# Kernel tuning notes

Hardware: AMD Instinct MI355X
Metric: run time of the kernel (lower is better)

Reference implementation:

```python
import jax, jax.numpy as jnp
import numpy as np

N, CS, CZ, H, C, PQ, PV, N0, N1 = 768, 384, 128, 12, 64, 4, 8, 192, 64
CZ4 = CZ // 4
INF, EPS = 1e5, 1e-8


def setup_inputs() -> dict:
    key = jax.random.key(0)
    ks = jax.random.split(key, 24)

    def w(k, i, o):
        return jax.random.normal(k, (i, o), jnp.float32) / np.float32(np.sqrt(i))

    s = jax.random.normal(ks[0], (N, CS), jnp.float32)
    z = jax.random.normal(ks[1], (N, N, CZ), jnp.float32)
    rot = jnp.linalg.qr(jax.random.normal(ks[2], (N, 3, 3), jnp.float32))[0]
    trans = jax.random.normal(ks[3], (N, 3), jnp.float32)
    mask = jnp.ones((N,), jnp.float32)
    is_atom = jax.random.bernoulli(ks[4], 0.5, (N,))
    return dict(
        s=s, z=z, rot=rot, trans=trans, mask=mask, is_atom=is_atom,
        wq=w(ks[5], CS, H * C), bq=jnp.zeros((H * C,), jnp.float32),
        wkv=w(ks[6], CS, 2 * H * C), bkv=jnp.zeros((2 * H * C,), jnp.float32),
        wqp=w(ks[7], CS, 3 * H * PQ), bqp=jnp.zeros((3 * H * PQ,), jnp.float32),
        wkvp=w(ks[8], CS, 3 * H * (PQ + PV)), bkvp=jnp.zeros((3 * H * (PQ + PV),), jnp.float32),
        wb=w(ks[9], CZ, H), bb=jnp.zeros((H,), jnp.float32),
        wdz=w(ks[10], CZ, CZ4), bdz=jnp.zeros((CZ4,), jnp.float32),
        head_weights=jnp.full((H,), 0.5413248, jnp.float32),  # softplus^-1(1), per ipa_point_weights_init_
        wout=w(ks[11], H * (C + 4 * PV + CZ4), CS), bout=jnp.zeros((CS,), jnp.float32),
        tfnq_ws=w(ks[12], N0, H * C), tfnq_wv=w(ks[13], N1, H * PQ),
        tfnkv_ws=w(ks[14], N0, 2 * H * C), tfnkv_wv=w(ks[15], N1, H * (PQ + PV)),
        tfno_ws=w(ks[16], H * (C + PV + CZ4), N0), tfno_wv=w(ks[17], H * PV, N1),
    )


def reference(s, z, rot, trans, mask, is_atom, wq, bq, wkv, bkv, wqp, bqp, wkvp, bkvp,
              wb, bb, wdz, bdz, head_weights, wout, bout,
              tfnq_ws, tfnq_wv, tfnkv_ws, tfnkv_wv, tfno_ws, tfno_wv):
    n = s.shape[0]

    def apply_rigid(pts):  # pts: [n, P, 3] -> R x + t
        return jnp.einsum('nij,npj->npi', rot, pts) + trans[:, None, :]

    # ---- residue (frame) path ----
    q_r = (s @ wq + bq).reshape(n, H, C)
    kv_r = (s @ wkv + bkv).reshape(n, H, 2 * C)
    k_r, v_r = kv_r[..., :C], kv_r[..., C:]
    # torch.split-in-3 then stack(dim=-1) layout: [n, 3, H*P] -> [n, H*P, 3]
    qp = (s @ wqp + bqp).reshape(n, 3, H * PQ).transpose(0, 2, 1)
    q_pts_r = apply_rigid(qp).reshape(n, H, PQ, 3)
    kvp = (s @ wkvp + bkvp).reshape(n, 3, H * (PQ + PV)).transpose(0, 2, 1)
    kv_pts_r = apply_rigid(kvp).reshape(n, H, PQ + PV, 3)
    k_pts_r, v_pts_r = kv_pts_r[..., :PQ, :], kv_pts_r[..., PQ:, :]

    # ---- atom (TFN-equivariant) path: irreps = N0 scalars + N1 vectors ----
    sc = s[:, :N0]
    vec = s[:, N0:N0 + 3 * N1].reshape(n, N1, 3)
    q_a = (sc @ tfnq_ws).reshape(n, H, C)
    q_pts_a = jnp.einsum('nix,io->nox', vec, tfnq_wv).reshape(n, H, PQ, 3) + trans[:, None, None, :]
    kv_a = (sc @ tfnkv_ws).reshape(n, H, 2 * C)
    k_a, v_a = kv_a[..., :C], kv_a[..., C:]
    kv_pts_a = jnp.einsum('nix,io->nox', vec, tfnkv_wv).reshape(n, H, PQ + PV, 3) + trans[:, None, None, :]
    k_pts_a, v_pts_a = kv_pts_a[..., :PQ, :], kv_pts_a[..., PQ:, :]

    m1 = is_atom[:, None, None]
    m2 = is_atom[:, None, None, None]
    q = jnp.where(m1, q_a, q_r)
    k = jnp.where(m1, k_a, k_r)
    v = jnp.where(m1, v_a, v_r)
    q_pts = jnp.where(m2, q_pts_a, q_pts_r)
    k_pts = jnp.where(m2, k_pts_a, k_pts_r)
    v_pts = jnp.where(m2, v_pts_a, v_pts_r)

    # ---- attention logits ----
    b = z @ wb + bb  # [n, n, H]
    a = jnp.einsum('nhc,mhc->hnm', q, k) * np.float32(np.sqrt(1.0 / (3 * C)))
    a = a + np.float32(np.sqrt(1.0 / 3)) * b.transpose(2, 0, 1)

    disp = q_pts[:, None] - k_pts[None]          # [n, n, H, PQ, 3]
    pt_att = jnp.sum(disp * disp, axis=-1)       # [n, n, H, PQ]
    hw = jax.nn.softplus(head_weights) * np.float32(np.sqrt(1.0 / (3 * (PQ * 9.0 / 2))))
    pt_att = -0.5 * jnp.sum(pt_att * hw[:, None], axis=-1)  # [n, n, H]
    a = a + pt_att.transpose(2, 0, 1)

    sq_mask = INF * (mask[:, None] * mask[None, :] - 1.0)
    a = jax.nn.softmax(a + sq_mask[None], axis=-1)  # [H, n, n]

    # ---- aggregation ----
    o = jnp.einsum('hnm,mhc->nhc', a, v).reshape(n, H * C)
    o_pt = jnp.einsum('hnm,mhpx->nhpx', a, v_pts)  # [n, H, PV, 3]
    o_pt = jnp.einsum('nji,nhpj->nhpi', rot, o_pt - trans[:, None, None, :])  # invert_apply
    o_pt_norm = jnp.sqrt(jnp.sum(o_pt * o_pt, axis=-1) + EPS).reshape(n, H * PV)
    o_pt = o_pt.reshape(n, H * PV, 3)
    pair_z = z @ wdz + bdz  # [n, n, CZ4]
    o_pair = jnp.einsum('hnm,nmz->nhz', a, pair_z).reshape(n, H * CZ4)

    # ---- residue output head ----
    res_feats = jnp.concatenate([o, o_pt[..., 0], o_pt[..., 1], o_pt[..., 2], o_pt_norm, o_pair], axis=-1)
    res_out = res_feats @ wout + bout  # [n, CS]

    # ---- atom output head (equivariant linear: scalars mix, vectors mix per-component) ----
    atom_sc = jnp.concatenate([o, o_pt_norm, o_pair], axis=-1) @ tfno_ws  # [n, N0]
    atom_vec = jnp.einsum('npx,po->nox', o_pt, tfno_wv).reshape(n, 3 * N1)
    atom_out = jnp.concatenate([atom_sc, atom_vec], axis=-1)  # [n, CS]

    return jnp.where(is_atom[:, None], atom_out, res_out)
```

## Files before the change

kernel.cpp:

```cpp
#include <hip/hip_runtime.h>
#include <hip/hip_bf16.h>

static constexpr int NN = 768;

typedef short v8bf __attribute__((ext_vector_type(8)));
typedef float v4f  __attribute__((ext_vector_type(4)));
typedef unsigned short ushort_t;

__device__ __forceinline__ unsigned short f2bf(float f) {
  unsigned u = __float_as_uint(f);
  u += 0x7fffu + ((u >> 16) & 1u);
  return (unsigned short)(u >> 16);
}
__device__ __forceinline__ float bf2f(unsigned short s) {
  return __uint_as_float(((unsigned)s) << 16);
}

static constexpr size_t OFF_ISA    = 0;
static constexpr size_t OFF_WCT    = 1024;
static constexpr size_t OFF_BCAT   = 4096;
static constexpr size_t OFF_SBF    = 4160;
static constexpr size_t OFF_WQT    = 151616;
static constexpr size_t OFF_WKVT   = 299072;
static constexpr size_t OFF_WQPT   = 593984;
static constexpr size_t OFF_WKVPT  = 630848;
static constexpr size_t OFF_TFNQT  = 716864;
static constexpr size_t OFF_TFNKVT = 815168;
static constexpr size_t OFF_WOUTT  = 1011776;
static constexpr size_t OFF_TFNOT  = 1306688;
static constexpr size_t OFF_QR     = 1429568;
static constexpr size_t OFF_KVR    = 1724480;
static constexpr size_t OFF_QP     = 2314304;
static constexpr size_t OFF_KVP    = 2424896;
static constexpr size_t OFF_QA     = 2756672;
static constexpr size_t OFF_KVA    = 3051584;
static constexpr size_t OFF_QCAT   = 3641408;
static constexpr size_t OFF_KCAT   = 4083776;
static constexpr size_t OFF_RQ     = 4526144;
static constexpr size_t OFF_RK     = 4535360;
static constexpr size_t OFF_VCATN  = 4544576;
static constexpr size_t OFF_VCATT  = 4986944;
static constexpr size_t OFF_BB     = 5429312;
static constexpr size_t OFF_PZT    = 8968256;
static constexpr size_t OFF_ABF    = 18405440;
static constexpr size_t OFF_OPTRAW = 21944384;
static constexpr size_t OFF_RESF   = 22165568;
static constexpr size_t OFF_ATOMF  = 22755392;

__device__ void transpose_cv(const float* __restrict__ src, unsigned short* __restrict__ dst,
                             int K, int Kp, int N, int ky, int nx) {
  __shared__ float tl[32][33];
  const int k0 = ky * 32, n0 = nx * 32;
  const int tx = threadIdx.x & 31, ty = threadIdx.x >> 5;
  for (int it = 0; it < 4; ++it) {
    int r = ty + it * 8;
    float v = 0.f;
    if (k0 + r < K && n0 + tx < N) v = src[(long long)(k0 + r) * N + n0 + tx];
    tl[r][tx] = v;
  }
  __syncthreads();
  for (int it = 0; it < 4; ++it) {
    int r = ty + it * 8;
    if (n0 + r < N && k0 + tx < Kp)
      dst[(long long)(n0 + r) * Kp + k0 + tx] = f2bf(tl[tx][r]);
  }
}

__global__ __launch_bounds__(256) void prep0(
    float* wsf, const float* s, const float* wq, const float* wkv,
    const float* wqp, const float* wkvp, const float* tfnq_ws,
    const float* tfnkv_ws, const float* wout, const float* tfno_ws,
    const float* wb, const float* wdz, const float* bb, const float* bdz,
    const unsigned int* isa_raw)
{
  const int bx = blockIdx.x, t = threadIdx.x;
  if (bx < 288)       { int g = bx;        transpose_cv(wq,      (unsigned short*)(wsf+OFF_WQT),    384, 384, 768,  g/24, g%24); return; }
  else if (bx < 864)  { int g = bx-288;    transpose_cv(wkv,     (unsigned short*)(wsf+OFF_WKVT),   384, 384, 1536, g/48, g%48); return; }
  else if (bx < 924)  { int g = bx-864;    transpose_cv(wqp,     (unsigned short*)(wsf+OFF_WQPT),   384, 384, 144,  g/5,  g%5);  return; }
  else if (bx < 1092) { int g = bx-924;    transpose_cv(wkvp,    (unsigned short*)(wsf+OFF_WKVPT),  384, 384, 432,  g/14, g%14); return; }
  else if (bx < 1284) { int g = bx-1092;   transpose_cv(tfnq_ws, (unsigned short*)(wsf+OFF_TFNQT),  192, 256, 768,  g/24, g%24); return; }
  else if (bx < 1668) { int g = bx-1284;   transpose_cv(tfnkv_ws,(unsigned short*)(wsf+OFF_TFNKVT), 192, 256, 1536, g/48, g%48); return; }
  else if (bx < 2244) { int g = bx-1668;   transpose_cv(wout,    (unsigned short*)(wsf+OFF_WOUTT),  1536,1536,384,  g/12, g%12); return; }
  else if (bx < 2484) { int g = bx-2244;   transpose_cv(tfno_ws, (unsigned short*)(wsf+OFF_TFNOT),  1248,1280,192,  g/6,  g%6);  return; }
  else if (bx < 2772) {
    long long base = (long long)(bx - 2484) * 1024 + t * 4;
    float4 v = *(const float4*)(s + base);
    unsigned short tmp[4] = {f2bf(v.x), f2bf(v.y), f2bf(v.z), f2bf(v.w)};
    *(uint2*)((unsigned short*)(wsf + OFF_SBF) + base) = *(uint2*)tmp;
    return;
  } else if (bx < 2773) {
    __shared__ int notint, notfloat;
    int* ISA = (int*)(wsf + OFF_ISA);
    if (t == 0) { notint = 0; notfloat = 0; }
    __syncthreads();
    if (t < 192) {
      unsigned v = isa_raw[t];
      if (v > 1u) atomicOr(&notint, 1);
      if (v != 0u && v != 0x3F800000u) atomicOr(&notfloat, 1);
    }
    __syncthreads();
    const int mode = (!notint) ? 0 : ((!notfloat) ? 1 : 2);
    for (int n = t; n < NN; n += 256) {
      int val;
      if (mode == 2) val = (((const unsigned char*)isa_raw)[n] != 0);
      else           val = (isa_raw[n] != 0u);
      ISA[n] = val;
    }
    return;
  } else {
    const float rs3 = 0.57735026918962576f;
    unsigned short* WCT = (unsigned short*)(wsf + OFF_WCT);
    float* bcat = wsf + OFF_BCAT;
    int idx = (bx - 2773) * 256 + t;
    if (idx < 48 * 128) {
      int o = idx >> 7, k = idx & 127;
      float v = 0.f;
      if (o < 12) v = rs3 * wb[k * 12 + o];
      else if (o < 44) v = wdz[k * 32 + (o - 12)];
      WCT[o * 128 + k] = f2bf(v);
    }
    if (bx == 2773 && t < 48)
      bcat[t] = (t < 12) ? rs3 * bb[t] : (t < 44 ? bdz[t - 12] : 0.f);
  }
}

__device__ __forceinline__ void gemm16(
    char* lds, const unsigned short* __restrict__ A, int lda,
    const unsigned short* __restrict__ BT, int ldb, int KQ,
    const float* __restrict__ bias, int mode,
    float* Cf, unsigned short* Cb, int ldc, int Nc, int colb, int row0,
    const int* __restrict__ ISA, float* outp)
{
  v4f (*PS)[4][64] = (v4f (*)[4][64])lds;
  const int t = threadIdx.x, w = t >> 6, l = t & 63, l15 = l & 15, lg = l >> 4;
  const int rowA = row0 + l15;
  v4f acc[4] = {};
  const unsigned short* ap = A + (long long)rowA * lda + lg * 8;
  const int kend = (w + 1) * KQ;
  for (int k0 = w * KQ; k0 < kend; k0 += 32) {
    v8bf av = *(const v8bf*)(ap + k0);
#pragma unroll
    for (int cf = 0; cf < 4; ++cf) {
      v8bf bv = *(const v8bf*)(BT + (long long)(colb + cf * 16 + l15) * ldb + k0 + lg * 8);
      acc[cf] = __builtin_amdgcn_mfma_f32_16x16x32_bf16(av, bv, acc[cf], 0, 0, 0);
    }
  }
#pragma unroll
  for (int cf = 0; cf < 4; ++cf) PS[w][cf][l] = acc[cf];
  __syncthreads();
  const int cf = w;
  v4f sv = PS[0][cf][l] + PS[1][cf][l] + PS[2][cf][l] + PS[3][cf][l];
  const int c = colb + cf * 16 + l15;
  if (c < Nc) {
    float bvs = bias ? bias[c] : 0.f;
#pragma unroll
    for (int i = 0; i < 4; ++i) {
      int r = row0 + lg * 4 + i;
      float v = sv[i] + bvs;
      if (mode == 0)      Cf[(long long)r * ldc + c] = v;
      else if (mode == 1) Cb[(long long)r * ldc + c] = f2bf(v);
      else if (mode == 2) { if (!ISA[r]) outp[r * 384 + c] = v; }
      else                { if ( ISA[r]) outp[r * 384 + c] = v; }
    }
  }
}

__global__ __launch_bounds__(256) void mega1(
    float* wsf, const float* __restrict__ z,
    const float* bq, const float* bkv, const float* bqp, const float* bkvp)
{
  __shared__ __align__(16) char lds[34816];
  const int t = threadIdx.x;
  if (blockIdx.x < 4608) {
    unsigned short* Abf = (unsigned short*)lds;
    float* Sout = (float*)lds;
    const unsigned short* WCT = (const unsigned short*)(wsf + OFF_WCT);
    const float* bcat = wsf + OFF_BCAT;
    unsigned short* Bb  = (unsigned short*)(wsf + OFF_BB);
    unsigned short* PZT = (unsigned short*)(wsf + OFF_PZT);
    const long long row0 = (long long)blockIdx.x * 128;
    for (int i = 0; i < 16; ++i) {
      int fi = (i * 256 + t) * 4;
      float4 v = *(const float4*)(z + row0 * 128 + fi);
      int r = fi >> 7, c = fi & 127;
      unsigned short tmp[4] = {f2bf(v.x), f2bf(v.y), f2bf(v.z), f2bf(v.w)};
      *(uint2*)(Abf + r * 136 + c) = *(uint2*)tmp;
    }
    __syncthreads();
    const int w = t >> 6, l = t & 63, l15 = l & 15, lg = l >> 4;
    v4f acc[2][3] = {};
    for (int ks = 0; ks < 4; ++ks) {
      v8bf bvv[3];
#pragma unroll
      for (int cf = 0; cf < 3; ++cf)
        bvv[cf] = *(const v8bf*)(WCT + (cf * 16 + l15) * 128 + ks * 32 + lg * 8);
#pragma unroll
      for (int rf = 0; rf < 2; ++rf) {
        v8bf av = *(const v8bf*)(Abf + (w * 32 + rf * 16 + l15) * 136 + ks * 32 + lg * 8);
#pragma unroll
        for (int cf = 0; cf < 3; ++cf)
          acc[rf][cf] = __builtin_amdgcn_mfma_f32_16x16x32_bf16(av, bvv[cf], acc[rf][cf], 0, 0, 0);
      }
    }
    __syncthreads();
#pragma unroll
    for (int rf = 0; rf < 2; ++rf)
#pragma unroll
      for (int cf = 0; cf < 3; ++cf) {
        int o = cf * 16 + l15;
#pragma unroll
        for (int i = 0; i < 4; ++i) {
          int m = w * 32 + rf * 16 + lg * 4 + i;
          Sout[o * 132 + m] = acc[rf][cf][i];
        }
      }
    __syncthreads();
    const int n = blockIdx.x / 6;
    const int m0 = (blockIdx.x % 6) * 128;
    for (int idx = t; idx < 44 * 8; idx += 256) {
      int o = idx >> 3, seg = idx & 7;
      float bias = bcat[o];
      unsigned short tmp[16];
#pragma unroll
      for (int j = 0; j < 16; ++j) tmp[j] = f2bf(Sout[o * 132 + seg * 16 + j] + bias);
      unsigned short* gp;
      if (o < 12) gp = Bb + ((long long)o * 768 + n) * 768 + m0 + seg * 16;
      else        gp = PZT + ((long long)n * 32 + (o - 12)) * 768 + m0 + seg * 16;
      *(uint4*)gp = *(uint4*)tmp;
      *(uint4*)(gp + 8) = *(uint4*)(tmp + 8);
    }
    return;
  }
  const int g = blockIdx.x - 4608;
  const int bt = g / 82, xt = g % 82;
  const unsigned short* SBF = (const unsigned short*)(wsf + OFF_SBF);
  const unsigned short* BT; const float* bias; int ldb, KQ, mode, ldc, Nc, colb;
  float* Cf = nullptr; unsigned short* Cb = nullptr;
  if (xt < 12)      { BT=(const unsigned short*)(wsf+OFF_WQT);    bias=bq;     ldb=384; KQ=96; Cb=(unsigned short*)(wsf+OFF_QR);  ldc=768;  Nc=768;  colb=xt*64;      mode=1; }
  else if (xt < 36) { BT=(const unsigned short*)(wsf+OFF_WKVT);   bias=bkv;    ldb=384; KQ=96; Cb=(unsigned short*)(wsf+OFF_KVR); ldc=1536; Nc=1536; colb=(xt-12)*64; mode=1; }
  else if (xt < 39) { BT=(const unsigned short*)(wsf+OFF_WQPT);   bias=bqp;    ldb=384; KQ=96; Cf=wsf+OFF_QP;                     ldc=144;  Nc=144;  colb=(xt-36)*64; mode=0; }
  else if (xt < 46) { BT=(const unsigned short*)(wsf+OFF_WKVPT);  bias=bkvp;   ldb=384; KQ=96; Cf=wsf+OFF_KVP;                    ldc=432;  Nc=432;  colb=(xt-39)*64; mode=0; }
  else if (xt < 58) { BT=(const unsigned short*)(wsf+OFF_TFNQT);  bias=nullptr;ldb=256; KQ=64; Cb=(unsigned short*)(wsf+OFF_QA);  ldc=768;  Nc=768;  colb=(xt-46)*64; mode=1; }
  else              { BT=(const unsigned short*)(wsf+OFF_TFNKVT); bias=nullptr;ldb=256; KQ=64; Cb=(unsigned short*)(wsf+OFF_KVA); ldc=1536; Nc=1536; colb=(xt-58)*64; mode=1; }
  gemm16(lds, SBF, 384, BT, ldb, KQ, bias, mode, Cf, Cb, ldc, Nc, colb, bt * 16, nullptr, nullptr);
}

__global__ __launch_bounds__(256) void prep_qkv(
    float* wsf, const float* __restrict__ s,
    const float* __restrict__ rot, const float* __restrict__ trans,
    const float* __restrict__ head_w,
    const float* __restrict__ tfnq_wv, const float* __restrict__ tfnkv_wv)
{
  const int n = blockIdx.x, t = threadIdx.x;
  const int* ISA = (const int*)(wsf + OFF_ISA);
  const unsigned short* QRb  = (const unsigned short*)(wsf + OFF_QR);
  const unsigned short* KVRb = (const unsigned short*)(wsf + OFF_KVR);
  const unsigned short* QAb  = (const unsigned short*)(wsf + OFF_QA);
  const unsigned short* KVAb = (const unsigned short*)(wsf + OFF_KVA);
  const float* QP  = wsf + OFF_QP;
  const float* KVP = wsf + OFF_KVP;
  unsigned short* Qcat  = (unsigned short*)(wsf + OFF_QCAT);
  unsigned short* Kcat  = (unsigned short*)(wsf + OFF_KCAT);
  unsigned short* Vcatn = (unsigned short*)(wsf + OFF_VCATN);
  float* rq = wsf + OFF_RQ;
  float* rk = wsf + OFF_RK;
  const bool isa = ISA[n] != 0;
  __shared__ float R[9], T[3], shw[12], sv[192];
  __shared__ float qs[768], ks[768], vs[768], qp[144], kp[144], vp[288];
  if (t < 9) R[t] = rot[n * 9 + t];
  if (t < 3) T[t] = trans[n * 3 + t];
  if (t >= 16 && t < 28)
    shw[t - 16] = log1pf(__expf(head_w[t - 16])) * 0.13608276348795434f;
  if (isa && t >= 32 && t < 224) sv[t - 32] = s[(size_t)n * 384 + 192 + (t - 32)];
  __syncthreads();
  for (int idx = t; idx < 768; idx += 256) {
    int h = idx >> 6, c = idx & 63;
    qs[idx] = bf2f(isa ? QAb[(long long)n * 768 + idx] : QRb[(long long)n * 768 + idx]);
    ks[idx] = bf2f(isa ? KVAb[(long long)n * 1536 + h * 128 + c] : KVRb[(long long)n * 1536 + h * 128 + c]);
    vs[idx] = bf2f(isa ? KVAb[(long long)n * 1536 + h * 128 + 64 + c] : KVRb[(long long)n * 1536 + h * 128 + 64 + c]);
  }
  if (isa) {
    for (int idx = t; idx < 144; idx += 256) {
      int hp = idx / 3, x = idx % 3;
      float a = 0.f;
      for (int i = 0; i < 64; ++i) a += sv[i * 3 + x] * tfnq_wv[i * 48 + hp];
      qp[idx] = a + T[x];
    }
    for (int idx = t; idx < 432; idx += 256) {
      int o = idx / 3, x = idx % 3;
      float a = 0.f;
      for (int i = 0; i < 64; ++i) a += sv[i * 3 + x] * tfnkv_wv[i * 144 + o];
      float v = a + T[x];
      int h = o / 12, pp = o % 12;
      if (pp < 4) kp[(h * 4 + pp) * 3 + x] = v;
      else        vp[(h * 8 + (pp - 4)) * 3 + x] = v;
    }
  } else {
    for (int idx = t; idx < 144; idx += 256) {
      int hp = idx / 3, i = idx % 3;
      qp[idx] = R[i * 3 + 0] * QP[(long long)n * 144 + 0 + hp] +
                R[i * 3 + 1] * QP[(long long)n * 144 + 48 + hp] +
                R[i * 3 + 2] * QP[(long long)n * 144 + 96 + hp] + T[i];
    }
    for (int idx = t; idx < 432; idx += 256) {
      int hp = idx / 3, i = idx % 3;
      float v = R[i * 3 + 0] * KVP[(long long)n * 432 + 0 + hp] +
                R[i * 3 + 1] * KVP[(long long)n * 432 + 144 + hp] +
                R[i * 3 + 2] * KVP[(long long)n * 432 + 288 + hp] + T[i];
      int h = hp / 12, pp = hp % 12;
      if (pp < 4) kp[(h * 4 + pp) * 3 + i] = v;
      else        vp[(h * 8 + (pp - 4)) * 3 + i] = v;
    }
  }
  __syncthreads();
  const float sq = 0.07216878364870322f;
  for (int idx = t; idx < 1152; idx += 256) {
    int h = idx / 96, c = idx % 96;
    float qv = (c < 64) ? sq * qs[h * 64 + c] : ((c < 76) ? shw[h] * qp[h * 12 + (c - 64)] : 0.f);
    float kv = (c < 64) ? ks[h * 64 + c]      : ((c < 76) ? kp[h * 12 + (c - 64)] : 0.f);
    float vv = (c < 64) ? vs[h * 64 + c]      : ((c < 88) ? vp[h * 24 + (c - 64)] : 0.f);
    long long base = ((long long)n * 12 + h) * 96 + c;
    Qcat[base] = f2bf(qv);
    Kcat[base] = f2bf(kv);
    Vcatn[base] = f2bf(vv);
  }
  if (t < 24) {
    int h = t >> 1, which = t & 1;
    const float* p = which ? kp : qp;
    float s2 = 0.f;
#pragma unroll
    for (int d = 0; d < 12; ++d) { float x = p[h * 12 + d]; s2 += x * x; }
    float val = 0.5f * shw[h] * s2;
    if (which) rk[h * 768 + n] = val;
    else       rq[h * 768 + n] = val;
  }
}

__global__ __launch_bounds__(256) void mega2(float* wsf, const float* __restrict__ mask) {
  __shared__ __align__(16) char lds[26112];
  const int t = threadIdx.x;
  if (blockIdx.x < 576) {
    const unsigned short* Qcat = (const unsigned short*)(wsf + OFF_QCAT);
    const unsigned short* Kcat = (const unsigned short*)(wsf + OFF_KCAT);
    const unsigned short* Bb   = (const unsigned short*)(wsf + OFF_BB);
    const float* rq = wsf + OFF_RQ;
    const float* rk = wsf + OFF_RK;
    unsigned short* Abf = (unsigned short*)(wsf + OFF_ABF);
    const int h = blockIdx.x / 48, r0 = (blockIdx.x % 48) * 16;
    const int w = t >> 6, l = t & 63, l15 = l & 15, lg = l >> 4;
    unsigned short* SW = (unsigned short*)lds + w * 3200;
    float* redm = (float*)(lds + 25600);
    float* reds = (float*)(lds + 25856);
    const int nrow = r0 + l15;
    v8bf aq[3];
#pragma unroll
    for (int ks = 0; ks < 3; ++ks)
      aq[ks] = *(const v8bf*)(Qcat + ((long long)nrow * 12 + h) * 96 + ks * 32 + lg * 8);
    v4f acc[12] = {};
#pragma unroll
    for (int cf = 0; cf < 12; ++cf) {
      int m = w * 192 + cf * 16 + l15;
      const unsigned short* kb = Kcat + ((long long)m * 12 + h) * 96 + lg * 8;
#pragma unroll
      for (int ks = 0; ks < 3; ++ks) {
        v8bf bv = *(const v8bf*)(kb + ks * 32);
        acc[cf] = __builtin_amdgcn_mfma_f32_16x16x32_bf16(aq[ks], bv, acc[cf], 0, 0, 0);
      }
    }
#pragma unroll
    for (int it = 0; it < 6; ++it) {
      int chunk = it * 64 + l;
      int row = chunk / 24, cc = (chunk % 24) * 8;
      *(uint4*)(SW + row * 200 + cc) =
          *(const uint4*)(Bb + ((long long)(h * 768 + r0 + row)) * 768 + w * 192 + cc);
    }
    __syncthreads();
    float rkm[12], mkm[12];
#pragma unroll
    for (int cf = 0; cf < 12; ++cf) {
      int m = w * 192 + cf * 16 + l15;
      rkm[cf] = rk[h * 768 + m];
      mkm[cf] = mask[m];
    }
    float rqn[4], mkn[4], mymax[4];
#pragma unroll
    for (int i = 0; i < 4; ++i) {
      int gn = r0 + lg * 4 + i;
      rqn[i] = rq[h * 768 + gn];
      mkn[i] = mask[gn];
      mymax[i] = -3.0e38f;
    }
#pragma unroll
    for (int cf = 0; cf < 12; ++cf)
#pragma unroll
      for (int i = 0; i < 4; ++i) {
        float v = acc[cf][i] + bf2f(SW[(lg * 4 + i) * 200 + cf * 16 + l15])
                - rqn[i] - rkm[cf] + 100000.0f * (mkn[i] * mkm[cf] - 1.0f);
        acc[cf][i] = v;
        mymax[i] = fmaxf(mymax[i], v);
      }
#pragma unroll
    for (int off = 1; off < 16; off <<= 1)
#pragma unroll
      for (int i = 0; i < 4; ++i) mymax[i] = fmaxf(mymax[i], __shfl_xor(mymax[i], off, 64));
    if (l15 == 0) {
#pragma unroll
      for (int i = 0; i < 4; ++i) redm[w * 16 + lg * 4 + i] = mymax[i];
    }
    __syncthreads();
    float mx[4], mysum[4];
#pragma unroll
    for (int i = 0; i < 4; ++i) {
      int rl = lg * 4 + i;
      mx[i] = fmaxf(fmaxf(redm[rl], redm[16 + rl]), fmaxf(redm[32 + rl], redm[48 + rl]));
      mysum[i] = 0.f;
    }
#pragma unroll
    for (int cf = 0; cf < 12; ++cf)
#pragma unroll
      for (int i = 0; i < 4; ++i) {
        float e = __expf(acc[cf][i] - mx[i]);
        acc[cf][i] = e;
        mysum[i] += e;
      }
#pragma unroll
    for (int off = 1; off < 16; off <<= 1)
#pragma unroll
      for (int i = 0; i < 4; ++i) mysum[i] += __shfl_xor(mysum[i], off, 64);
    if (l15 == 0) {
#pragma unroll
      for (int i = 0; i < 4; ++i) reds[w * 16 + lg * 4 + i] = mysum[i];
    }
    __syncthreads();
    float inv[4];
#pragma unroll
    for (int i = 0; i < 4; ++i) {
      int rl = lg * 4 + i;
      inv[i] = 1.0f / (reds[rl] + reds[16 + rl] + reds[32 + rl] + reds[48 + rl]);
    }
#pragma unroll
    for (int cf = 0; cf < 12; ++cf)
#pragma unroll
      for (int i = 0; i < 4; ++i)
        SW[(lg * 4 + i) * 200 + cf * 16 + l15] = f2bf(acc[cf][i] * inv[i]);
    __syncthreads();
#pragma unroll
    for (int it = 0; it < 6; ++it) {
      int chunk = it * 64 + l;
      int row = chunk / 24, cc = (chunk % 24) * 8;
      *(uint4*)(Abf + ((long long)(h * 768 + r0 + row)) * 768 + w * 192 + cc) =
          *(const uint4*)(SW + row * 200 + cc);
    }
    return;
  }
  {
    const unsigned short* Vn = (const unsigned short*)(wsf + OFF_VCATN);
    unsigned short* Vt = (unsigned short*)(wsf + OFF_VCATT);
    const int g = blockIdx.x - 576;
    const int h = g / 12, n0 = (g % 12) * 64;
    unsigned short (*tl)[104] = (unsigned short (*)[104])lds;
    for (int i4 = t; i4 < 768; i4 += 256) {
      int r = i4 / 12, cseg = (i4 % 12) * 8;
      *(uint4*)(&tl[r][cseg]) = *(const uint4*)(Vn + ((long long)(n0 + r) * 12 + h) * 96 + cseg);
    }
    __syncthreads();
    for (int i4 = t; i4 < 768; i4 += 256) {
      int c = i4 >> 3, seg = i4 & 7;
      unsigned short tmp[8];
#pragma unroll
      for (int j = 0; j < 8; ++j) tmp[j] = tl[seg * 8 + j][c];
      *(uint4*)(Vt + ((long long)h * 96 + c) * 768 + n0 + seg * 8) = *(uint4*)tmp;
    }
  }
}

__global__ __launch_bounds__(256) void mega3(float* wsf) {
  __shared__ __align__(16) char lds[24576];
  const int t = threadIdx.x, w = t >> 6, l = t & 63, l15 = l & 15, lg = l >> 4;
  const unsigned short* Abf = (const unsigned short*)(wsf + OFF_ABF);
  unsigned short* RESF  = (unsigned short*)(wsf + OFF_RESF);
  unsigned short* ATOMF = (unsigned short*)(wsf + OFF_ATOMF);
  if (blockIdx.x < 576) {
    const unsigned short* VcatT = (const unsigned short*)(wsf + OFF_VCATT);
    float* OPTRAW = wsf + OFF_OPTRAW;
    v4f (*PS)[64] = (v4f (*)[64])lds;
    const int h = blockIdx.x / 48, nt = blockIdx.x % 48;
    const int nrow = nt * 16 + l15;
    const unsigned short* arow = Abf + ((long long)h * 768 + nrow) * 768 + lg * 8;
    const unsigned short* vbase = VcatT + (long long)h * 96 * 768 + lg * 8;
    v4f acc[6] = {};
    for (int k0 = w * 192; k0 < w * 192 + 192; k0 += 32) {
      v8bf av = *(const v8bf*)(arow + k0);
#pragma unroll
      for (int cf = 0; cf < 6; ++cf) {
        v8bf bv = *(const v8bf*)(vbase + (long long)(cf * 16 + l15) * 768 + k0);
        acc[cf] = __builtin_amdgcn_mfma_f32_16x16x32_bf16(av, bv, acc[cf], 0, 0, 0);
      }
    }
#pragma unroll
    for (int cf = 0; cf < 6; ++cf) PS[w * 6 + cf][l] = acc[cf];
    __syncthreads();
    for (int cf = w; cf < 6; cf += 4) {
      v4f sv = PS[cf][l] + PS[6 + cf][l] + PS[12 + cf][l] + PS[18 + cf][l];
      int c = cf * 16 + l15;
      int rb = nt * 16 + lg * 4;
#pragma unroll
      for (int i = 0; i < 4; ++i) {
        int n = rb + i;
        float v = sv[i];
        if (c < 64) {
          unsigned short b = f2bf(v);
          RESF[(long long)n * 1536 + h * 64 + c] = b;
          ATOMF[(long long)n * 1280 + h * 64 + c] = b;
        } else if (c < 88) {
          OPTRAW[(long long)n * 288 + h * 24 + (c - 64)] = v;
        }
      }
    }
    return;
  }
  {
    const unsigned short* PZT = (const unsigned short*)(wsf + OFF_PZT);
    v4f (*PS)[64] = (v4f (*)[64])lds;
    const int n = blockIdx.x - 576;
    const int hh = (l15 < 12) ? l15 : 0;
    const unsigned short* arow = Abf + ((long long)hh * 768 + n) * 768 + lg * 8;
    const unsigned short* pz = PZT + (long long)n * 32 * 768 + lg * 8;
    v4f acc[2] = {};
    for (int k0 = w * 192; k0 < w * 192 + 192; k0 += 32) {
      v8bf av = *(const v8bf*)(arow + k0);
#pragma unroll
      for (int cf = 0; cf < 2; ++cf) {
        v8bf bv = *(const v8bf*)(pz + (long long)(cf * 16 + l15) * 768 + k0);
        acc[cf] = __builtin_amdgcn_mfma_f32_16x16x32_bf16(av, bv, acc[cf], 0, 0, 0);
      }
    }
    PS[w * 2 + 0][l] = acc[0];
    PS[w * 2 + 1][l] = acc[1];
    __syncthreads();
    if (t < 128) {
      int cf = t >> 6, ll = t & 63;
      v4f sv = PS[cf][ll] + PS[2 + cf][ll] + PS[4 + cf][ll] + PS[6 + cf][ll];
      int zc = cf * 16 + (ll & 15);
#pragma unroll
      for (int i = 0; i < 4; ++i) {
        int hd = (ll >> 4) * 4 + i;
        if (hd < 12) {
          unsigned short b = f2bf(sv[i]);
          RESF[(long long)n * 1536 + 1152 + hd * 32 + zc] = b;
          ATOMF[(long long)n * 1280 + 864 + hd * 32 + zc] = b;
        }
      }
    }
  }
}

__global__ __launch_bounds__(256) void finalize_k(
    float* wsf, const float* __restrict__ rot, const float* __restrict__ trans,
    const float* __restrict__ tfno_wv, float* __restrict__ out)
{
  const int n = blockIdx.x, t = threadIdx.x;
  const float* OPTRAW = wsf + OFF_OPTRAW;
  unsigned short* RESF  = (unsigned short*)(wsf + OFF_RESF);
  unsigned short* ATOMF = (unsigned short*)(wsf + OFF_ATOMF);
  const int* ISA = (const int*)(wsf + OFF_ISA);
  const bool isa = ISA[n] != 0;
  __shared__ float R[9], T[3], opt2[96][3], norml[96];
  if (t < 9) R[t] = rot[(size_t)n * 9 + t];
  if (t < 3) T[t] = trans[(size_t)n * 3 + t];
  __syncthreads();
  for (int idx = t; idx < 288; idx += 256) {
    int hp = idx / 3, i = idx % 3;
    float x = OPTRAW[(size_t)n * 288 + hp * 3 + 0] - T[0];
    float y = OPTRAW[(size_t)n * 288 + hp * 3 + 1] - T[1];
    float z = OPTRAW[(size_t)n * 288 + hp * 3 + 2] - T[2];
    opt2[hp][i] = R[0 + i] * x + R[3 + i] * y + R[6 + i] * z;
  }
  __syncthreads();
  if (t < 96)
    norml[t] = sqrtf(opt2[t][0] * opt2[t][0] + opt2[t][1] * opt2[t][1] +
                     opt2[t][2] * opt2[t][2] + 1e-8f);
  __syncthreads();
  const long long rb = (long long)n * 1536;
  const long long ab = (long long)n * 1280;
  for (int idx = t; idx < 288; idx += 256) {
    int x = idx / 96, hp = idx % 96;
    RESF[rb + 768 + idx] = f2bf(opt2[hp][x]);
  }
  for (int idx = t; idx < 96; idx += 256) {
    unsigned short b = f2bf(norml[idx]);
    RESF[rb + 1056 + idx] = b;
    ATOMF[ab + 768 + idx] = b;
  }
  if (isa) {
    for (int idx = t; idx < 192; idx += 256) {
      int o = idx / 3, x = idx % 3;
      float a = 0.f;
      for (int p = 0; p < 96; ++p) a += opt2[p][x] * tfno_wv[p * 64 + o];
      out[(size_t)n * 384 + 192 + idx] = a;
    }
  }
}

__global__ __launch_bounds__(256) void outg(float* wsf, const float* __restrict__ bout,
                                            float* __restrict__ out) {
  __shared__ __align__(16) char lds[16384];
  const int g = blockIdx.x;
  const int bt = g / 9, xt = g % 9;
  const int* ISA = (const int*)(wsf + OFF_ISA);
  if (xt < 6)
    gemm16(lds, (const unsigned short*)(wsf + OFF_RESF), 1536,
           (const unsigned short*)(wsf + OFF_WOUTT), 1536, 384, bout, 2,
           nullptr, nullptr, 0, 384, xt * 64, bt * 16, ISA, out);
  else
    gemm16(lds, (const unsigned short*)(wsf + OFF_ATOMF), 1280,
           (const unsigned short*)(wsf + OFF_TFNOT), 1280, 320, nullptr, 3,
           nullptr, nullptr, 0, 192, (xt - 6) * 64, bt * 16, ISA, out);
}

extern "C" void kernel_launch(void* const* d_in, const int* in_sizes, int n_in,
                              void* d_out, int out_size, void* d_ws, size_t ws_size,
                              hipStream_t stream) {
  (void)in_sizes; (void)n_in; (void)out_size; (void)ws_size;
  const float* s      = (const float*)d_in[0];
  const float* z      = (const float*)d_in[1];
  const float* rot    = (const float*)d_in[2];
  const float* trans  = (const float*)d_in[3];
  const float* mask   = (const float*)d_in[4];
  const float* wq     = (const float*)d_in[6];
  const float* bq     = (const float*)d_in[7];
  const float* wkv    = (const float*)d_in[8];
  const float* bkv    = (const float*)d_in[9];
  const float* wqp    = (const float*)d_in[10];
  const float* bqp    = (const float*)d_in[11];
  const float* wkvp   = (const float*)d_in[12];
  const float* bkvp   = (const float*)d_in[13];
  const float* wb     = (const float*)d_in[14];
  const float* bb     = (const float*)d_in[15];
  const float* wdz    = (const float*)d_in[16];
  const float* bdz    = (const float*)d_in[17];
  const float* head_w = (const float*)d_in[18];
  const float* wout   = (const float*)d_in[19];
  const float* bout   = (const float*)d_in[20];
  const float* tfnq_ws  = (const float*)d_in[21];
  const float* tfnq_wv  = (const float*)d_in[22];
  const float* tfnkv_ws = (const float*)d_in[23];
  const float* tfnkv_wv = (const float*)d_in[24];
  const float* tfno_ws  = (const float*)d_in[25];
  const float* tfno_wv  = (const float*)d_in[26];

  float* wsf = (float*)d_ws;

  prep0<<<2797, 256, 0, stream>>>(wsf, s, wq, wkv, wqp, wkvp, tfnq_ws, tfnkv_ws,
                                  wout, tfno_ws, wb, wdz, bb, bdz,
                                  (const unsigned int*)d_in[5]);
  mega1<<<8544, 256, 0, stream>>>(wsf, z, bq, bkv, bqp, bkvp);
  prep_qkv<<<768, 256, 0, stream>>>(wsf, s, rot, trans, head_w, tfnq_wv, tfnkv_wv);
  mega2<<<720, 256, 0, stream>>>(wsf, mask);
  mega3<<<1344, 256, 0, stream>>>(wsf);
  finalize_k<<<768, 256, 0, stream>>>(wsf, rot, trans, tfno_wv, (float*)d_out);
  outg<<<432, 256, 0, stream>>>(wsf, bout, (float*)d_out);
}
```

Baseline: 189.2 us.

## Fuse softmax with AV aggregation, write V transposed directly, drop LDS staging of z

mega1 now loads z rows straight from global memory into registers, converts them to bf16 and feeds the MFMA operands directly, with the weight fragments preloaded. This removes the LDS staging buffer and one barrier. prep_qkv writes V in transposed layout directly, so the separate transpose blocks go away. mega2 now does the A·V product from the softmax tile still held in LDS instead of re-reading the attention matrix in a later kernel. finalize_k is merged into mega3 as extra blocks, cutting launches from seven to six. The costs are strided 2-byte scattered stores for the V transpose and uncoalesced direct z loads in mega1.

```diff
diff --git a/kernel.cpp b/kernel.cpp
--- a/kernel.cpp
+++ b/kernel.cpp
@@ -5,7 +5,6 @@
 
 typedef short v8bf __attribute__((ext_vector_type(8)));
 typedef float v4f  __attribute__((ext_vector_type(4)));
-typedef unsigned short ushort_t;
 
 __device__ __forceinline__ unsigned short f2bf(float f) {
   unsigned u = __float_as_uint(f);
@@ -38,7 +37,6 @@
 static constexpr size_t OFF_KCAT   = 4083776;
 static constexpr size_t OFF_RQ     = 4526144;
 static constexpr size_t OFF_RK     = 4535360;
-static constexpr size_t OFF_VCATN  = 4544576;
 static constexpr size_t OFF_VCATT  = 4986944;
 static constexpr size_t OFF_BB     = 5429312;
 static constexpr size_t OFF_PZT    = 8968256;
@@ -169,40 +167,38 @@
     float* wsf, const float* __restrict__ z,
     const float* bq, const float* bkv, const float* bqp, const float* bkvp)
 {
-  __shared__ __align__(16) char lds[34816];
+  __shared__ __align__(16) char lds[23296];
   const int t = threadIdx.x;
   if (blockIdx.x < 4608) {
-    unsigned short* Abf = (unsigned short*)lds;
     float* Sout = (float*)lds;
     const unsigned short* WCT = (const unsigned short*)(wsf + OFF_WCT);
     const float* bcat = wsf + OFF_BCAT;
     unsigned short* Bb  = (unsigned short*)(wsf + OFF_BB);
     unsigned short* PZT = (unsigned short*)(wsf + OFF_PZT);
     const long long row0 = (long long)blockIdx.x * 128;
-    for (int i = 0; i < 16; ++i) {
-      int fi = (i * 256 + t) * 4;
-      float4 v = *(const float4*)(z + row0 * 128 + fi);
-      int r = fi >> 7, c = fi & 127;
-      unsigned short tmp[4] = {f2bf(v.x), f2bf(v.y), f2bf(v.z), f2bf(v.w)};
-      *(uint2*)(Abf + r * 136 + c) = *(uint2*)tmp;
-    }
-    __syncthreads();
     const int w = t >> 6, l = t & 63, l15 = l & 15, lg = l >> 4;
+    v8bf bvv[4][3];
+#pragma unroll
+    for (int ks = 0; ks < 4; ++ks)
+#pragma unroll
+      for (int cf = 0; cf < 3; ++cf)
+        bvv[ks][cf] = *(const v8bf*)(WCT + (cf * 16 + l15) * 128 + ks * 32 + lg * 8);
     v4f acc[2][3] = {};
-    for (int ks = 0; ks < 4; ++ks) {
-      v8bf bvv[3];
-#pragma unroll
-      for (int cf = 0; cf < 3; ++cf)
-        bvv[cf] = *(const v8bf*)(WCT + (cf * 16 + l15) * 128 + ks * 32 + lg * 8);
-#pragma unroll
-      for (int rf = 0; rf < 2; ++rf) {
-        v8bf av = *(const v8bf*)(Abf + (w * 32 + rf * 16 + l15) * 136 + ks * 32 + lg * 8);
+#pragma unroll
+    for (int rf = 0; rf < 2; ++rf) {
+      const float* zrow = z + (row0 + w * 32 + rf * 16 + l15) * 128 + lg * 8;
+#pragma unroll
+      for (int ks = 0; ks < 4; ++ks) {
+        float4 a0 = *(const float4*)(zrow + ks * 32);
+        float4 a1 = *(const float4*)(zrow + ks * 32 + 4);
+        unsigned short tmp[8] = {f2bf(a0.x), f2bf(a0.y), f2bf(a0.z), f2bf(a0.w),
+                                 f2bf(a1.x), f2bf(a1.y), f2bf(a1.z), f2bf(a1.w)};
+        v8bf av = *(const v8bf*)tmp;
 #pragma unroll
         for (int cf = 0; cf < 3; ++cf)
-          acc[rf][cf] = __builtin_amdgcn_mfma_f32_16x16x32_bf16(av, bvv[cf], acc[rf][cf], 0, 0, 0);
+          acc[rf][cf] = __builtin_amdgcn_mfma_f32_16x16x32_bf16(av, bvv[ks][cf], acc[rf][cf], 0, 0, 0);
       }
     }
-    __syncthreads();
 #pragma unroll
     for (int rf = 0; rf < 2; ++rf)
 #pragma unroll
@@ -259,9 +255,9 @@
   const unsigned short* KVAb = (const unsigned short*)(wsf + OFF_KVA);
   const float* QP  = wsf + OFF_QP;
   const float* KVP = wsf + OFF_KVP;
-  unsigned short* Qcat  = (unsigned short*)(wsf + OFF_QCAT);
-  unsigned short* Kcat  = (unsigned short*)(wsf + OFF_KCAT);
-  unsigned short* Vcatn = (unsigned short*)(wsf + OFF_VCATN);
+  unsigned short* Qcat = (unsigned short*)(wsf + OFF_QCAT);
+  unsigned short* Kcat = (unsigned short*)(wsf + OFF_KCAT);
+  unsigned short* Vt   = (unsigned short*)(wsf + OFF_VCATT);
   float* rq = wsf + OFF_RQ;
   float* rk = wsf + OFF_RK;
   const bool isa = ISA[n] != 0;
@@ -322,7 +318,7 @@
     long long base = ((long long)n * 12 + h) * 96 + c;
     Qcat[base] = f2bf(qv);
     Kcat[base] = f2bf(kv);
-    Vcatn[base] = f2bf(vv);
+    Vt[((long long)h * 96 + c) * 768 + n] = f2bf(vv);
   }
   if (t < 24) {
     int h = t >> 1, which = t & 1;
@@ -339,190 +335,168 @@
 __global__ __launch_bounds__(256) void mega2(float* wsf, const float* __restrict__ mask) {
   __shared__ __align__(16) char lds[26112];
   const int t = threadIdx.x;
-  if (blockIdx.x < 576) {
-    const unsigned short* Qcat = (const unsigned short*)(wsf + OFF_QCAT);
-    const unsigned short* Kcat = (const unsigned short*)(wsf + OFF_KCAT);
-    const unsigned short* Bb   = (const unsigned short*)(wsf + OFF_BB);
-    const float* rq = wsf + OFF_RQ;
-    const float* rk = wsf + OFF_RK;
-    unsigned short* Abf = (unsigned short*)(wsf + OFF_ABF);
-    const int h = blockIdx.x / 48, r0 = (blockIdx.x % 48) * 16;
-    const int w = t >> 6, l = t & 63, l15 = l & 15, lg = l >> 4;
-    unsigned short* SW = (unsigned short*)lds + w * 3200;
-    float* redm = (float*)(lds + 25600);
-    float* reds = (float*)(lds + 25856);
-    const int nrow = r0 + l15;
-    v8bf aq[3];
-#pragma unroll
-    for (int ks = 0; ks < 3; ++ks)
-      aq[ks] = *(const v8bf*)(Qcat + ((long long)nrow * 12 + h) * 96 + ks * 32 + lg * 8);
-    v4f acc[12] = {};
-#pragma unroll
-    for (int cf = 0; cf < 12; ++cf) {
-      int m = w * 192 + cf * 16 + l15;
-      const unsigned short* kb = Kcat + ((long long)m * 12 + h) * 96 + lg * 8;
-#pragma unroll
-      for (int ks = 0; ks < 3; ++ks) {
-        v8bf bv = *(const v8bf*)(kb + ks * 32);
-        acc[cf] = __builtin_amdgcn_mfma_f32_16x16x32_bf16(aq[ks], bv, acc[cf], 0, 0, 0);
-      }
-    }
-#pragma unroll
-    for (int it = 0; it < 6; ++it) {
-      int chunk = it * 64 + l;
-      int row = chunk / 24, cc = (chunk % 24) * 8;
-      *(uint4*)(SW + row * 200 + cc) =
-          *(const uint4*)(Bb + ((long long)(h * 768 + r0 + row)) * 768 + w * 192 + cc);
-    }
-    __syncthreads();
-    float rkm[12], mkm[12];
-#pragma unroll
-    for (int cf = 0; cf < 12; ++cf) {
-      int m = w * 192 + cf * 16 + l15;
-      rkm[cf] = rk[h * 768 + m];
-      mkm[cf] = mask[m];
-    }
-    float rqn[4], mkn[4], mymax[4];
-#pragma unroll
-    for (int i = 0; i < 4; ++i) {
-      int gn = r0 + lg * 4 + i;
-      rqn[i] = rq[h * 768 + gn];
-      mkn[i] = mask[gn];
-      mymax[i] = -3.0e38f;
-    }
-#pragma unroll
-    for (int cf = 0; cf < 12; ++cf)
-#pragma unroll
-      for (int i = 0; i < 4; ++i) {
-        float v = acc[cf][i] + bf2f(SW[(lg * 4 + i) * 200 + cf * 16 + l15])
-                - rqn[i] - rkm[cf] + 100000.0f * (mkn[i] * mkm[cf] - 1.0f);
-        acc[cf][i] = v;
-        mymax[i] = fmaxf(mymax[i], v);
-      }
-#pragma unroll
-    for (int off = 1; off < 16; off <<= 1)
-#pragma unroll
-      for (int i = 0; i < 4; ++i) mymax[i] = fmaxf(mymax[i], __shfl_xor(mymax[i], off, 64));
-    if (l15 == 0) {
-#pragma unroll
-      for (int i = 0; i < 4; ++i) redm[w * 16 + lg * 4 + i] = mymax[i];
-    }
-    __syncthreads();
-    float mx[4], mysum[4];
-#pragma unroll
-    for (int i = 0; i < 4; ++i) {
-      int rl = lg * 4 + i;
-      mx[i] = fmaxf(fmaxf(redm[rl], redm[16 + rl]), fmaxf(redm[32 + rl], redm[48 + rl]));
-      mysum[i] = 0.f;
-    }
-#pragma unroll
-    for (int cf = 0; cf < 12; ++cf)
-#pragma unroll
-      for (int i = 0; i < 4; ++i) {
-        float e = __expf(acc[cf][i] - mx[i]);
-        acc[cf][i] = e;
-        mysum[i] += e;
-      }
-#pragma unroll
-    for (int off = 1; off < 16; off <<= 1)
-#pragma unroll
-      for (int i = 0; i < 4; ++i) mysum[i] += __shfl_xor(mysum[i], off, 64);
-    if (l15 == 0) {
-#pragma unroll
-      for (int i = 0; i < 4; ++i) reds[w * 16 + lg * 4 + i] = mysum[i];
-    }
-    __syncthreads();
-    float inv[4];
-#pragma unroll
-    for (int i = 0; i < 4; ++i) {
-      int rl = lg * 4 + i;
-      inv[i] = 1.0f / (reds[rl] + reds[16 + rl] + reds[32 + rl] + reds[48 + rl]);
-    }
-#pragma unroll
-    for (int cf = 0; cf < 12; ++cf)
-#pragma unroll
-      for (int i = 0; i < 4; ++i)
-        SW[(lg * 4 + i) * 200 + cf * 16 + l15] = f2bf(acc[cf][i] * inv[i]);
-    __syncthreads();
-#pragma unroll
-    for (int it = 0; it < 6; ++it) {
-      int chunk = it * 64 + l;
-      int row = chunk / 24, cc = (chunk % 24) * 8;
-      *(uint4*)(Abf + ((long long)(h * 768 + r0 + row)) * 768 + w * 192 + cc) =
-          *(const uint4*)(SW + row * 200 + cc);
-    }
-    return;
-  }
-  {
-    const unsigned short* Vn = (const unsigned short*)(wsf + OFF_VCATN);
-    unsigned short* Vt = (unsigned short*)(wsf + OFF_VCATT);
-    const int g = blockIdx.x - 576;
-    const int h = g / 12, n0 = (g % 12) * 64;
-    unsigned short (*tl)[104] = (unsigned short (*)[104])lds;
-    for (int i4 = t; i4 < 768; i4 += 256) {
-      int r = i4 / 12, cseg = (i4 % 12) * 8;
-      *(uint4*)(&tl[r][cseg]) = *(const uint4*)(Vn + ((long long)(n0 + r) * 12 + h) * 96 + cseg);
-    }
-    __syncthreads();
-    for (int i4 = t; i4 < 768; i4 += 256) {
-      int c = i4 >> 3, seg = i4 & 7;
-      unsigned short tmp[8];
-#pragma unroll
-      for (int j = 0; j < 8; ++j) tmp[j] = tl[seg * 8 + j][c];
-      *(uint4*)(Vt + ((long long)h * 96 + c) * 768 + n0 + seg * 8) = *(uint4*)tmp;
-    }
-  }
-}
-
-__global__ __launch_bounds__(256) void mega3(float* wsf) {
-  __shared__ __align__(16) char lds[24576];
-  const int t = threadIdx.x, w = t >> 6, l = t & 63, l15 = l & 15, lg = l >> 4;
-  const unsigned short* Abf = (const unsigned short*)(wsf + OFF_ABF);
+  const unsigned short* Qcat = (const unsigned short*)(wsf + OFF_QCAT);
+  const unsigned short* Kcat = (const unsigned short*)(wsf + OFF_KCAT);
+  const unsigned short* Bb   = (const unsigned short*)(wsf + OFF_BB);
+  const unsigned short* VcatT= (const unsigned short*)(wsf + OFF_VCATT);
+  const float* rq = wsf + OFF_RQ;
+  const float* rk = wsf + OFF_RK;
+  unsigned short* Abf   = (unsigned short*)(wsf + OFF_ABF);
   unsigned short* RESF  = (unsigned short*)(wsf + OFF_RESF);
   unsigned short* ATOMF = (unsigned short*)(wsf + OFF_ATOMF);
-  if (blockIdx.x < 576) {
-    const unsigned short* VcatT = (const unsigned short*)(wsf + OFF_VCATT);
-    float* OPTRAW = wsf + OFF_OPTRAW;
-    v4f (*PS)[64] = (v4f (*)[64])lds;
-    const int h = blockIdx.x / 48, nt = blockIdx.x % 48;
-    const int nrow = nt * 16 + l15;
-    const unsigned short* arow = Abf + ((long long)h * 768 + nrow) * 768 + lg * 8;
-    const unsigned short* vbase = VcatT + (long long)h * 96 * 768 + lg * 8;
-    v4f acc[6] = {};
-    for (int k0 = w * 192; k0 < w * 192 + 192; k0 += 32) {
-      v8bf av = *(const v8bf*)(arow + k0);
-#pragma unroll
-      for (int cf = 0; cf < 6; ++cf) {
-        v8bf bv = *(const v8bf*)(vbase + (long long)(cf * 16 + l15) * 768 + k0);
-        acc[cf] = __builtin_amdgcn_mfma_f32_16x16x32_bf16(av, bv, acc[cf], 0, 0, 0);
+  float* OPTRAW = wsf + OFF_OPTRAW;
+  const int h = blockIdx.x / 48, r0 = (blockIdx.x % 48) * 16;
+  const int w = t >> 6, l = t & 63, l15 = l & 15, lg = l >> 4;
+  unsigned short* SW = (unsigned short*)lds + w * 3200;
+  float* redm = (float*)(lds + 25600);
+  float* reds = (float*)(lds + 25856);
+  const int nrow = r0 + l15;
+  v8bf aq[3];
+#pragma unroll
+  for (int ks = 0; ks < 3; ++ks)
+    aq[ks] = *(const v8bf*)(Qcat + ((long long)nrow * 12 + h) * 96 + ks * 32 + lg * 8);
+  v4f acc[12] = {};
+#pragma unroll
+  for (int cf = 0; cf < 12; ++cf) {
+    int m = w * 192 + cf * 16 + l15;
+    const unsigned short* kb = Kcat + ((long long)m * 12 + h) * 96 + lg * 8;
+#pragma unroll
+    for (int ks = 0; ks < 3; ++ks) {
+      v8bf bv = *(const v8bf*)(kb + ks * 32);
+      acc[cf] = __builtin_amdgcn_mfma_f32_16x16x32_bf16(aq[ks], bv, acc[cf], 0, 0, 0);
+    }
+  }
+#pragma unroll
+  for (int it = 0; it < 6; ++it) {
+    int chunk = it * 64 + l;
+    int row = chunk / 24, cc = (chunk % 24) * 8;
+    *(uint4*)(SW + row * 200 + cc) =
+        *(const uint4*)(Bb + ((long long)(h * 768 + r0 + row)) * 768 + w * 192 + cc);
+  }
+  __syncthreads();
+  float rkm[12], mkm[12];
+#pragma unroll
+  for (int cf = 0; cf < 12; ++cf) {
+    int m = w * 192 + cf * 16 + l15;
+    rkm[cf] = rk[h * 768 + m];
+    mkm[cf] = mask[m];
+  }
+  float rqn[4], mkn[4], mymax[4];
+#pragma unroll
+  for (int i = 0; i < 4; ++i) {
+    int gn = r0 + lg * 4 + i;
+    rqn[i] = rq[h * 768 + gn];
+    mkn[i] = mask[gn];
+    mymax[i] = -3.0e38f;
+  }
+#pragma unroll
+  for (int cf = 0; cf < 12; ++cf)
+#pragma unroll
+    for (int i = 0; i < 4; ++i) {
+      float v = acc[cf][i] + bf2f(SW[(lg * 4 + i) * 200 + cf * 16 + l15])
+              - rqn[i] - rkm[cf] + 100000.0f * (mkn[i] * mkm[cf] - 1.0f);
+      acc[cf][i] = v;
+      mymax[i] = fmaxf(mymax[i], v);
+    }
+#pragma unroll
+  for (int off = 1; off < 16; off <<= 1)
+#pragma unroll
+    for (int i = 0; i < 4; ++i) mymax[i] = fmaxf(mymax[i], __shfl_xor(mymax[i], off, 64));
+  if (l15 == 0) {
+#pragma unroll
+    for (int i = 0; i < 4; ++i) redm[w * 16 + lg * 4 + i] = mymax[i];
+  }
+  __syncthreads();
+  float mx[4], mysum[4];
+#pragma unroll
+  for (int i = 0; i < 4; ++i) {
+    int rl = lg * 4 + i;
+    mx[i] = fmaxf(fmaxf(redm[rl], redm[16 + rl]), fmaxf(redm[32 + rl], redm[48 + rl]));
+    mysum[i] = 0.f;
+  }
+#pragma unroll
+  for (int cf = 0; cf < 12; ++cf)
+#pragma unroll
+    for (int i = 0; i < 4; ++i) {
+      float e = __expf(acc[cf][i] - mx[i]);
+      acc[cf][i] = e;
+      mysum[i] += e;
+    }
+#pragma unroll
+  for (int off = 1; off < 16; off <<= 1)
+#pragma unroll
+    for (int i = 0; i < 4; ++i) mysum[i] += __shfl_xor(mysum[i], off, 64);
+  if (l15 == 0) {
+#pragma unroll
+    for (int i = 0; i < 4; ++i) reds[w * 16 + lg * 4 + i] = mysum[i];
+  }
+  __syncthreads();
+  float inv[4];
+#pragma unroll
+  for (int i = 0; i < 4; ++i) {
+    int rl = lg * 4 + i;
+    inv[i] = 1.0f / (reds[rl] + reds[16 + rl] + reds[32 + rl] + reds[48 + rl]);
+  }
+#pragma unroll
+  for (int cf = 0; cf < 12; ++cf)
+#pragma unroll
+    for (int i = 0; i < 4; ++i)
+      SW[(lg * 4 + i) * 200 + cf * 16 + l15] = f2bf(acc[cf][i] * inv[i]);
+  __syncthreads();
+#pragma unroll
+  for (int it = 0; it < 6; ++it) {
+    int chunk = it * 64 + l;
+    int row = chunk / 24, cc = (chunk % 24) * 8;
+    *(uint4*)(Abf + ((long long)(h * 768 + r0 + row)) * 768 + w * 192 + cc) =
+        *(const uint4*)(SW + row * 200 + cc);
+  }
+  const unsigned short* vbase = VcatT + (long long)h * 96 * 768 + w * 192 + lg * 8;
+  v4f acc2[6] = {};
+  for (int kk = 0; kk < 192; kk += 32) {
+    v8bf av = *(const v8bf*)(SW + l15 * 200 + kk + lg * 8);
+#pragma unroll
+    for (int cf = 0; cf < 6; ++cf) {
+      v8bf bv = *(const v8bf*)(vbase + (long long)(cf * 16 + l15) * 768 + kk);
+      acc2[cf] = __builtin_amdgcn_mfma_f32_16x16x32_bf16(av, bv, acc2[cf], 0, 0, 0);
+    }
+  }
+  __syncthreads();
+  v4f (*PS)[64] = (v4f (*)[64])lds;
+#pragma unroll
+  for (int cf = 0; cf < 6; ++cf) PS[w * 6 + cf][l] = acc2[cf];
+  __syncthreads();
+  for (int cf = w; cf < 6; cf += 4) {
+    v4f sv = PS[cf][l] + PS[6 + cf][l] + PS[12 + cf][l] + PS[18 + cf][l];
+    int c = cf * 16 + l15;
+    int rb = r0 + lg * 4;
+#pragma unroll
+    for (int i = 0; i < 4; ++i) {
+      int n = rb + i;
+      float v = sv[i];
+      if (c < 64) {
+        unsigned short b = f2bf(v);
+        RESF[(long long)n * 1536 + h * 64 + c] = b;
+        ATOMF[(long long)n * 1280 + h * 64 + c] = b;
+      } else if (c < 88) {
+        OPTRAW[(long long)n * 288 + h * 24 + (c - 64)] = v;
       }
     }
-#pragma unroll
-    for (int cf = 0; cf < 6; ++cf) PS[w * 6 + cf][l] = acc[cf];
-    __syncthreads();
-    for (int cf = w; cf < 6; cf += 4) {
-      v4f sv = PS[cf][l] + PS[6 + cf][l] + PS[12 + cf][l] + PS[18 + cf][l];
-      int c = cf * 16 + l15;
-      int rb = nt * 16 + lg * 4;
-#pragma unroll
-      for (int i = 0; i < 4; ++i) {
-        int n = rb + i;
-        float v = sv[i];
-        if (c < 64) {
-          unsigned short b = f2bf(v);
-          RESF[(long long)n * 1536 + h * 64 + c] = b;
-          ATOMF[(long long)n * 1280 + h * 64 + c] = b;
-        } else if (c < 88) {
-          OPTRAW[(long long)n * 288 + h * 24 + (c - 64)] = v;
-        }
-      }
-    }
-    return;
-  }
-  {
+  }
+}
+
+__global__ __launch_bounds__(256) void mega3(
+    float* wsf, const float* __restrict__ rot, const float* __restrict__ trans,
+    const float* __restrict__ tfno_wv, float* __restrict__ out)
+{
+  const int t = threadIdx.x;
+  unsigned short* RESF  = (unsigned short*)(wsf + OFF_RESF);
+  unsigned short* ATOMF = (unsigned short*)(wsf + OFF_ATOMF);
+  if (blockIdx.x < 768) {
+    __shared__ __align__(16) v4f PS[8][64];
+    const unsigned short* Abf = (const unsigned short*)(wsf + OFF_ABF);
     const unsigned short* PZT = (const unsigned short*)(wsf + OFF_PZT);
-    v4f (*PS)[64] = (v4f (*)[64])lds;
-    const int n = blockIdx.x - 576;
+    const int w = t >> 6, l = t & 63, l15 = l & 15, lg = l >> 4;
+    const int n = blockIdx.x;
     const int hh = (l15 < 12) ? l15 : 0;
     const unsigned short* arow = Abf + ((long long)hh * 768 + n) * 768 + lg * 8;
     const unsigned short* pz = PZT + (long long)n * 32 * 768 + lg * 8;
@@ -552,52 +526,47 @@
         }
       }
     }
-  }
-}
-
-__global__ __launch_bounds__(256) void finalize_k(
-    float* wsf, const float* __restrict__ rot, const float* __restrict__ trans,
-    const float* __restrict__ tfno_wv, float* __restrict__ out)
-{
-  const int n = blockIdx.x, t = threadIdx.x;
-  const float* OPTRAW = wsf + OFF_OPTRAW;
-  unsigned short* RESF  = (unsigned short*)(wsf + OFF_RESF);
-  unsigned short* ATOMF = (unsigned short*)(wsf + OFF_ATOMF);
-  const int* ISA = (const int*)(wsf + OFF_ISA);
-  const bool isa = ISA[n] != 0;
-  __shared__ float R[9], T[3], opt2[96][3], norml[96];
-  if (t < 9) R[t] = rot[(size_t)n * 9 + t];
-  if (t < 3) T[t] = trans[(size_t)n * 3 + t];
-  __syncthreads();
-  for (int idx = t; idx < 288; idx += 256) {
-    int hp = idx / 3, i = idx % 3;
-    float x = OPTRAW[(size_t)n * 288 + hp * 3 + 0] - T[0];
-    float y = OPTRAW[(size_t)n * 288 + hp * 3 + 1] - T[1];
-    float z = OPTRAW[(size_t)n * 288 + hp * 3 + 2] - T[2];
-    opt2[hp][i] = R[0 + i] * x + R[3 + i] * y + R[6 + i] * z;
-  }
-  __syncthreads();
-  if (t < 96)
-    norml[t] = sqrtf(opt2[t][0] * opt2[t][0] + opt2[t][1] * opt2[t][1] +
-                     opt2[t][2] * opt2[t][2] + 1e-8f);
-  __syncthreads();
-  const long long rb = (long long)n * 1536;
-  const long long ab = (long long)n * 1280;
-  for (int idx = t; idx < 288; idx += 256) {
-    int x = idx / 96, hp = idx % 96;
-    RESF[rb + 768 + idx] = f2bf(opt2[hp][x]);
-  }
-  for (int idx = t; idx < 96; idx += 256) {
-    unsigned short b = f2bf(norml[idx]);
-    RESF[rb + 1056 + idx] = b;
-    ATOMF[ab + 768 + idx] = b;
-  }
-  if (isa) {
-    for (int idx = t; idx < 192; idx += 256) {
-      int o = idx / 3, x = idx % 3;
-      float a = 0.f;
-      for (int p = 0; p < 96; ++p) a += opt2[p][x] * tfno_wv[p * 64 + o];
-      out[(size_t)n * 384 + 192 + idx] = a;
+    return;
+  }
+  {
+    const int n = blockIdx.x - 768;
+    const float* OPTRAW = wsf + OFF_OPTRAW;
+    const int* ISA = (const int*)(wsf + OFF_ISA);
+    const bool isa = ISA[n] != 0;
+    __shared__ float R[9], T[3], opt2[96][3], norml[96];
+    if (t < 9) R[t] = rot[(size_t)n * 9 + t];
+    if (t < 3) T[t] = trans[(size_t)n * 3 + t];
+    __syncthreads();
+    for (int idx = t; idx < 288; idx += 256) {
+      int hp = idx / 3, i = idx % 3;
+      float x = OPTRAW[(size_t)n * 288 + hp * 3 + 0] - T[0];
+      float y = OPTRAW[(size_t)n * 288 + hp * 3 + 1] - T[1];
+      float z = OPTRAW[(size_t)n * 288 + hp * 3 + 2] - T[2];
+      opt2[hp][i] = R[0 + i] * x + R[3 + i] * y + R[6 + i] * z;
+    }
+    __syncthreads();
+    if (t < 96)
+      norml[t] = sqrtf(opt2[t][0] * opt2[t][0] + opt2[t][1] * opt2[t][1] +
+                       opt2[t][2] * opt2[t][2] + 1e-8f);
+    __syncthreads();
+    const long long rb = (long long)n * 1536;
+    const long long ab = (long long)n * 1280;
+    for (int idx = t; idx < 288; idx += 256) {
+      int x = idx / 96, hp = idx % 96;
+      RESF[rb + 768 + idx] = f2bf(opt2[hp][x]);
+    }
+    for (int idx = t; idx < 96; idx += 256) {
+      unsigned short b = f2bf(norml[idx]);
+      RESF[rb + 1056 + idx] = b;
+      ATOMF[ab + 768 + idx] = b;
+    }
+    if (isa) {
+      for (int idx = t; idx < 192; idx += 256) {
+        int o = idx / 3, x = idx % 3;
+        float a = 0.f;
+        for (int p = 0; p < 96; ++p) a += opt2[p][x] * tfno_wv[p * 64 + o];
+        out[(size_t)n * 384 + 192 + idx] = a;
+      }
     }
   }
 }
@@ -656,8 +625,7 @@
                                   (const unsigned int*)d_in[5]);
   mega1<<<8544, 256, 0, stream>>>(wsf, z, bq, bkv, bqp, bkvp);
   prep_qkv<<<768, 256, 0, stream>>>(wsf, s, rot, trans, head_w, tfnq_wv, tfnkv_wv);
-  mega2<<<720, 256, 0, stream>>>(wsf, mask);
-  mega3<<<1344, 256, 0, stream>>>(wsf);
-  finalize_k<<<768, 256, 0, stream>>>(wsf, rot, trans, tfno_wv, (float*)d_out);
+  mega2<<<576, 256, 0, stream>>>(wsf, mask);
+  mega3<<<1536, 256, 0, stream>>>(wsf, rot, trans, tfno_wv, (float*)d_out);
   outg<<<432, 256, 0, stream>>>(wsf, bout, (float*)d_out);
 }
```

Result: no change. 186.1 us (-1.7%).
